# Kernel optimization log

Hardware: AMD Instinct MI355X
Metric: run time of the kernel (lower is better)

The kernel has to match this reference:

```python
import math
import jax, jax.numpy as jnp
import numpy as np


def conv2d(x, w, b, pad=0, dil=1):
    # x: [B, Cin, H, W], w: [Cout, Cin, kh, kw] (OIHW)
    y = jax.lax.conv_general_dilated(
        x, w, window_strides=(1, 1),
        padding=[(pad, pad), (pad, pad)],
        rhs_dilation=(dil, dil),
        dimension_numbers=('NCHW', 'OIHW', 'NCHW'))
    return y + b[None, :, None, None]


def setup_inputs() -> dict:
    key = jax.random.key(0)
    ks = jax.random.split(key, 8)
    B, C, H, W = 2, 64, 96, 96
    inner = 64 // 18  # = 3, as in the torch module
    n_dil = 3
    s = 0.1
    x = jax.random.normal(ks[0], (B, C, H, W), jnp.float32)
    w_red = jax.random.normal(ks[1], (inner, C, 1, 1), jnp.float32) * s
    b_red = jax.random.normal(ks[2], (inner,), jnp.float32) * s
    w_dil = jax.random.normal(ks[3], (n_dil, inner, inner, 3, 3), jnp.float32) * s
    b_dil = jax.random.normal(ks[4], (n_dil, inner), jnp.float32) * s
    w_fuse = jax.random.normal(ks[5], (C, inner * n_dil * 6, 1, 1), jnp.float32) * s
    b_fuse = jax.random.normal(ks[6], (C,), jnp.float32) * s
    return {"x": x, "w_red": w_red, "b_red": b_red, "w_dil": w_dil,
            "b_dil": b_dil, "w_fuse": w_fuse, "b_fuse": b_fuse}


def _c4_transforms(x):
    # identity, flip-W, flip-H, rot90 k=1,2,3 over spatial dims
    return [x,
            jnp.flip(x, axis=-1),
            jnp.flip(x, axis=-2),
            jnp.rot90(x, 1, axes=(2, 3)),
            jnp.rot90(x, 2, axes=(2, 3)),
            jnp.rot90(x, 3, axes=(2, 3))]


def reference(x, w_red, b_red, w_dil, b_dil, w_fuse, b_fuse):
    dilations = (1, 2, 3)
    residual_scale = 0.2
    B, C, H, W = x.shape
    x_red = conv2d(x, w_red, b_red)                    # [B, inner, H, W]
    tfs = _c4_transforms(x_red)
    feats = []
    for i, d in enumerate(dilations):
        co = conv2d(x_red, w_dil[i], b_dil[i], pad=d, dil=d)
        for tf in tfs:
            feats.append(co * tf)
    cat = jnp.concatenate(feats, axis=1)               # [B, inner*18, H, W]
    fused = conv2d(cat, w_fuse, b_fuse)                # [B, C, H, W]
    tokens = fused.reshape(B, C, H * W).transpose(0, 2, 1)  # [B, N, C]
    # Chunked attention in the original is mathematically full self-attention
    scores = jnp.einsum('bnc,bmc->bnm', tokens, tokens) / math.sqrt(C)
    attn = jax.nn.softmax(scores, axis=-1)
    out = jnp.einsum('bnm,bmc->bnc', attn, tokens)     # [B, N, C]
    out = out.transpose(0, 2, 1).reshape(B, C, H, W)
    return x + residual_scale * out
```

## Files before the change

### kernel.cpp

```cpp
#include <hip/hip_runtime.h>

#define HW    96
#define NPIX  9216
#define NCH   64
#define INNER 3
#define NDIL  3
#define BB    2
#define TOTPIX (BB * NPIX)
#define NT32  (NPIX / 32)

typedef __attribute__((ext_vector_type(8))) short short8;
typedef __attribute__((ext_vector_type(8))) unsigned short ushort8;
typedef __attribute__((ext_vector_type(4))) float f32x4;
typedef __attribute__((ext_vector_type(4))) unsigned int uint32x4;

__device__ __forceinline__ ushort f2bf_rne(float f) {
    unsigned u = __float_as_uint(f);
    u += 0x7fffu + ((u >> 16) & 1u);
    return (ushort)(u >> 16);
}
__device__ __forceinline__ float bf2f(ushort u) {
    return __uint_as_float((unsigned)u << 16);
}
__device__ __forceinline__ unsigned pack_bf(float lo, float hi) {
    return __builtin_amdgcn_perm(__float_as_uint(hi), __float_as_uint(lo), 0x07060302u);
}

__global__ __launch_bounds__(256) void
k_reduce(const float* __restrict__ x, const float* __restrict__ w_red,
         const float* __restrict__ b_red, float* __restrict__ xred) {
    __shared__ float part[4][3][64];
    int tid = threadIdx.x;
    int cp = tid >> 6, lane = tid & 63;
    int pix = blockIdx.x * 64 + lane;
    int b = pix / NPIX, n = pix % NPIX;
    const float* xb = x + (size_t)b * NCH * NPIX + (size_t)(cp * 16) * NPIX + n;
    float a0 = 0.f, a1 = 0.f, a2 = 0.f;
    #pragma unroll
    for (int c = 0; c < 16; ++c) {
        float xv = xb[(size_t)c * NPIX];
        a0 = fmaf(w_red[0 * NCH + cp * 16 + c], xv, a0);
        a1 = fmaf(w_red[1 * NCH + cp * 16 + c], xv, a1);
        a2 = fmaf(w_red[2 * NCH + cp * 16 + c], xv, a2);
    }
    part[cp][0][lane] = a0; part[cp][1][lane] = a1; part[cp][2][lane] = a2;
    __syncthreads();
    if (tid < 192) {
        int o = tid >> 6, lp = tid & 63;
        float s = ((part[0][o][lp] + part[1][o][lp]) +
                   (part[2][o][lp] + part[3][o][lp])) + b_red[o];
        int pix2 = blockIdx.x * 64 + lp;
        int b2 = pix2 / NPIX, n2 = pix2 % NPIX;
        xred[((size_t)b2 * INNER + o) * NPIX + n2] = s;
    }
}

__global__ __launch_bounds__(256) void
k_feat(const float* __restrict__ xred, const float* __restrict__ w_dil,
       const float* __restrict__ b_dil, ushort* __restrict__ FT) {
    int gid = blockIdx.x * 256 + threadIdx.x;
    int io = gid / TOTPIX;
    int pix = gid - io * TOTPIX;
    int i3 = io / 3, o = io - 3 * i3;
    int b = pix / NPIX, n = pix % NPIX;
    int h = n / HW, w = n % HW;
    const float* xr = xred + (size_t)b * INNER * NPIX;
    int d = i3 + 1;

    float co = b_dil[i3 * 3 + o];
    #pragma unroll
    for (int ci = 0; ci < 3; ++ci) {
        const float* xo = xr + ci * NPIX;
        #pragma unroll
        for (int kh = 0; kh < 3; ++kh) {
            int hh = h + (kh - 1) * d;
            #pragma unroll
            for (int kw = 0; kw < 3; ++kw) {
                int ww = w + (kw - 1) * d;
                float v = ((unsigned)hh < HW && (unsigned)ww < HW) ? xo[hh * HW + ww] : 0.f;
                co = fmaf(w_dil[(9 * i3 + 3 * o + ci) * 9 + kh * 3 + kw], v, co);
            }
        }
    }

    const float* xo = xr + o * NPIX;
    float tf0 = xo[h * HW + w];
    float tf1 = xo[h * HW + (HW - 1 - w)];
    float tf2 = xo[(HW - 1 - h) * HW + w];
    float tf3 = xo[w * HW + (HW - 1 - h)];
    float tf4 = xo[(HW - 1 - h) * HW + (HW - 1 - w)];
    float tf5 = xo[(HW - 1 - w) * HW + h];

    size_t base = (size_t)(i3 * 18 + o) * TOTPIX + pix;
    FT[base + (size_t)(0 * 3) * TOTPIX] = f2bf_rne(co * tf0);
    FT[base + (size_t)(1 * 3) * TOTPIX] = f2bf_rne(co * tf1);
    FT[base + (size_t)(2 * 3) * TOTPIX] = f2bf_rne(co * tf2);
    FT[base + (size_t)(3 * 3) * TOTPIX] = f2bf_rne(co * tf3);
    FT[base + (size_t)(4 * 3) * TOTPIX] = f2bf_rne(co * tf4);
    FT[base + (size_t)(5 * 3) * TOTPIX] = f2bf_rne(co * tf5);
}

__global__ __launch_bounds__(256) void
k_fuse(const ushort* __restrict__ FT, const float* __restrict__ w_fuse,
       const float* __restrict__ b_fuse, ushort* __restrict__ tok,
       ushort* __restrict__ tokTt) {
    __shared__ ushort wpad[64 * 72];
    __shared__ float  bsh[64];
    __shared__ ushort tile[64 * 72];

    int tid = threadIdx.x;
    for (int i = tid; i < 64 * 64; i += 256) {
        int c = i >> 6, j = i & 63;
        wpad[c * 72 + j] = (j < 54) ? f2bf_rne(w_fuse[c * 54 + j]) : (ushort)0;
    }
    if (tid < 64) bsh[tid] = b_fuse[tid];
    __syncthreads();

    int wv = tid >> 6, lane = tid & 63, quad = lane >> 4, l15 = lane & 15;
    int px0 = blockIdx.x * 64;

    short8 af[4][2];
    #pragma unroll
    for (int m = 0; m < 4; ++m)
        #pragma unroll
        for (int kc = 0; kc < 2; ++kc)
            af[m][kc] = *(const short8*)&wpad[(16 * m + l15) * 72 + quad * 8 + 32 * kc];

    f32x4 acc[4];
    #pragma unroll
    for (int m = 0; m < 4; ++m) acc[m] = (f32x4){0.f, 0.f, 0.f, 0.f};

    int px = px0 + wv * 16 + l15;
    #pragma unroll
    for (int kc = 0; kc < 2; ++kc) {
        short8 bf;
        #pragma unroll
        for (int jj = 0; jj < 8; ++jj)
            bf[jj] = (short)FT[(size_t)(quad * 8 + jj + 32 * kc) * TOTPIX + px];
        #pragma unroll
        for (int m = 0; m < 4; ++m)
            acc[m] = __builtin_amdgcn_mfma_f32_16x16x32_bf16(af[m][kc], bf, acc[m], 0, 0, 0);
    }

    #pragma unroll
    for (int m = 0; m < 4; ++m)
        #pragma unroll
        for (int r = 0; r < 4; ++r) {
            int c = 16 * m + quad * 4 + r;
            tile[c * 72 + wv * 16 + l15] = f2bf_rne(acc[m][r] + bsh[c]);
        }
    __syncthreads();

    int b0 = px0 / NPIX, n0 = px0 % NPIX;
    {
        int lp = tid >> 2, part = tid & 3;
        ushort row[16];
        #pragma unroll
        for (int k = 0; k < 16; ++k) row[k] = tile[(part * 16 + k) * 72 + lp];
        ushort* dst = tok + ((size_t)b0 * NPIX + n0 + lp) * NCH + part * 16;
        *(ushort8*)&dst[0] = *(const ushort8*)&row[0];
        *(ushort8*)&dst[8] = *(const ushort8*)&row[8];
    }
    {
        int c = tid >> 2, seg = tid & 3;
        int n = n0 + seg * 16;
        size_t base = (((size_t)b0 * NT32 + (n >> 5)) * 64 + c) * 32 + (n & 31);
        *(ushort8*)&tokTt[base]     = *(const ushort8*)&tile[c * 72 + seg * 16];
        *(ushort8*)&tokTt[base + 8] = *(const ushort8*)&tile[c * 72 + seg * 16 + 8];
    }
}

__global__ __launch_bounds__(256, 4) void
k_attn(const ushort* __restrict__ tok, const ushort* __restrict__ tokTt,
       float* __restrict__ pl, ushort* __restrict__ pacc, int P, int KP) {
    __shared__ ushort ldsK[2][32 * 72];
    __shared__ ushort ldsV[2][64 * 40];

    const int QW = NPIX / 128;
    int bid = blockIdx.x;
    int qc = bid % QW; int rest = bid / QW;
    int p = rest % P;  int b = rest / P;
    int tid = threadIdx.x;
    int wv = tid >> 6, lane = tid & 63;
    int quad = lane >> 4, l15 = lane & 15;

    const ushort* tb  = tok + (size_t)b * NPIX * NCH;
    const ushort* tvb = tokTt + (size_t)b * NT32 * (64 * 32);
    int qwave = qc * 128 + wv * 32;

    int sk_off = (tid >> 3) * 72 + (tid & 7) * 8;
    int svj = tid & 3;
    int sv_b0 = (tid >> 2) * 40 + 8 * ((2 * svj) & 3) + 4 * (svj >> 1);
    int sv_b1 = (tid >> 2) * 40 + 8 * ((2 * svj + 1) & 3) + 4 * (svj >> 1);

    short8 qf[2][2];
    const float scale = 0.125f * 1.44269504088896340736f;
    #pragma unroll
    for (int n = 0; n < 2; ++n) {
        const ushort* qr = tb + (size_t)(qwave + 16 * n + l15) * NCH + quad * 8;
        #pragma unroll
        for (int kc = 0; kc < 2; ++kc) {
            ushort8 raw = *(const ushort8*)(qr + 32 * kc);
            short8 f;
            #pragma unroll
            for (int e = 0; e < 8; ++e) f[e] = (short)f2bf_rne(bf2f(raw[e]) * scale);
            qf[n][kc] = f;
        }
    }

    f32x4 O[4][2];
    #pragma unroll
    for (int m = 0; m < 4; ++m)
        #pragma unroll
        for (int n = 0; n < 2; ++n) O[m][n] = (f32x4){0.f, 0.f, 0.f, 0.f};
    float lrun[2] = {0.f, 0.f};

    const float FM = 16.0f;
    int k0 = p * KP;
    int nt = KP / 32;

    {
        ushort8 gK = *(const ushort8*)(tb + (size_t)k0 * NCH + tid * 8);
        ushort8 gV = *(const ushort8*)(tvb + ((size_t)(k0 >> 5)) * 2048 + tid * 8);
        *(ushort8*)&ldsK[0][sk_off] = gK;
        uint32x4 v4 = *(uint32x4*)&gV;
        *(uint2*)&ldsV[0][sv_b0] = make_uint2(v4.x, v4.y);
        *(uint2*)&ldsV[0][sv_b1] = make_uint2(v4.z, v4.w);
    }
    __syncthreads();

    for (int t = 0; t < nt; ++t) {
        int cur = t & 1;
        int kbase = k0 + t * 32;
        bool pre = (t + 1 < nt);

        ushort8 nK, nV;
        if (pre) {
            nK = *(const ushort8*)(tb + (size_t)(kbase + 32) * NCH + tid * 8);
            nV = *(const ushort8*)(tvb + ((size_t)((kbase + 32) >> 5)) * 2048 + tid * 8);
        }

        short8 kd[4];
        #pragma unroll
        for (int m2 = 0; m2 < 2; ++m2)
            #pragma unroll
            for (int kc = 0; kc < 2; ++kc)
                kd[2 * m2 + kc] = *(const short8*)&ldsK[cur][(16 * m2 + l15) * 72 +
                                                            quad * 8 + 32 * kc];

        f32x4 S[2][2];
        #pragma unroll
        for (int m = 0; m < 2; ++m)
            #pragma unroll
            for (int n = 0; n < 2; ++n) S[m][n] = (f32x4){0.f, 0.f, 0.f, 0.f};

        __builtin_amdgcn_s_setprio(1);
        #pragma unroll
        for (int m2 = 0; m2 < 2; ++m2)
            #pragma unroll
            for (int cc = 0; cc < 2; ++cc)
                #pragma unroll
                for (int n = 0; n < 2; ++n)
                    S[m2][n] = __builtin_amdgcn_mfma_f32_16x16x32_bf16(kd[2 * m2 + cc],
                                                                       qf[n][cc], S[m2][n],
                                                                       0, 0, 0);
        __builtin_amdgcn_s_setprio(0);

        if (pre) {
            *(ushort8*)&ldsK[cur ^ 1][sk_off] = nK;
            uint32x4 v4 = *(uint32x4*)&nV;
            *(uint2*)&ldsV[cur ^ 1][sv_b0] = make_uint2(v4.x, v4.y);
            *(uint2*)&ldsV[cur ^ 1][sv_b1] = make_uint2(v4.z, v4.w);
        }

        short8 vf[4];
        #pragma unroll
        for (int mc = 0; mc < 4; ++mc)
            vf[mc] = *(const short8*)&ldsV[cur][(16 * mc + l15) * 40 + quad * 8];

        #pragma unroll
        for (int n = 0; n < 2; ++n) {
            float e00 = __builtin_amdgcn_exp2f(S[0][n][0] - FM);
            float e01 = __builtin_amdgcn_exp2f(S[0][n][1] - FM);
            float e02 = __builtin_amdgcn_exp2f(S[0][n][2] - FM);
            float e03 = __builtin_amdgcn_exp2f(S[0][n][3] - FM);
            float e10 = __builtin_amdgcn_exp2f(S[1][n][0] - FM);
            float e11 = __builtin_amdgcn_exp2f(S[1][n][1] - FM);
            float e12 = __builtin_amdgcn_exp2f(S[1][n][2] - FM);
            float e13 = __builtin_amdgcn_exp2f(S[1][n][3] - FM);
            lrun[n] += ((e00 + e01) + (e02 + e03)) + ((e10 + e11) + (e12 + e13));
            uint32x4 w;
            w.x = pack_bf(e00, e01); w.y = pack_bf(e02, e03);
            w.z = pack_bf(e10, e11); w.w = pack_bf(e12, e13);
            short8 bfr = *(short8*)&w;

            __builtin_amdgcn_s_setprio(1);
            #pragma unroll
            for (int mc = 0; mc < 4; ++mc)
                O[mc][n] = __builtin_amdgcn_mfma_f32_16x16x32_bf16(vf[mc], bfr,
                                                                   O[mc][n], 0, 0, 0);
            __builtin_amdgcn_s_setprio(0);
        }

        __syncthreads();
    }

    #pragma unroll
    for (int n = 0; n < 2; ++n) {
        lrun[n] += __shfl_xor(lrun[n], 16, 64);
        lrun[n] += __shfl_xor(lrun[n], 32, 64);
    }
    size_t bp = (size_t)b * P + p;
    if (quad == 0) {
        #pragma unroll
        for (int n = 0; n < 2; ++n)
            pl[bp * NPIX + qwave + 16 * n + l15] = lrun[n];
    }
    #pragma unroll
    for (int n = 0; n < 2; ++n) {
        int qg = qwave + 16 * n + l15;
        #pragma unroll
        for (int m = 0; m < 4; ++m) {
            #pragma unroll
            for (int r = 0; r < 4; ++r) {
                int c = 16 * m + quad * 4 + r;
                pacc[(bp * NCH + c) * NPIX + qg] = f2bf_rne(O[m][n][r]);
            }
        }
    }
}

__global__ void k_norm(const float* __restrict__ pl, float* __restrict__ linv, int P) {
    int idx = blockIdx.x * blockDim.x + threadIdx.x;
    if (idx >= TOTPIX) return;
    int b = idx / NPIX, n = idx % NPIX;
    float L = 0.f;
    for (int p = 0; p < P; ++p) L += pl[((size_t)b * P + p) * NPIX + n];
    linv[idx] = 0.2f / L;
}

__global__ void k_combine(const float* __restrict__ x, const float* __restrict__ linv,
                          const ushort* __restrict__ pacc, float* __restrict__ out,
                          int P) {
    int gid = blockIdx.x * blockDim.x + threadIdx.x;
    if (gid >= BB * NCH * (NPIX / 8)) return;
    int seg = gid % (NPIX / 8);
    int bc  = gid / (NPIX / 8);
    int b = bc / NCH;
    int n0 = seg * 8;
    float o[8] = {0.f, 0.f, 0.f, 0.f, 0.f, 0.f, 0.f, 0.f};
    for (int p = 0; p < P; ++p) {
        ushort8 t = *(const ushort8*)(pacc +
            (((size_t)b * P + p) * NCH + (bc % NCH)) * NPIX + n0);
        #pragma unroll
        for (int e = 0; e < 8; ++e) o[e] += bf2f(t[e]);
    }
    const float* lv = linv + (size_t)b * NPIX + n0;
    const float* xb = x + (size_t)bc * NPIX + n0;
    float* ob = out + (size_t)bc * NPIX + n0;
    #pragma unroll
    for (int e = 0; e < 8; ++e)
        ob[e] = fmaf(lv[e], o[e], xb[e]);
}

extern "C" void kernel_launch(void* const* d_in, const int* in_sizes, int n_in,
                              void* d_out, int out_size, void* d_ws, size_t ws_size,
                              hipStream_t stream) {
    const float* x      = (const float*)d_in[0];
    const float* w_red  = (const float*)d_in[1];
    const float* b_red  = (const float*)d_in[2];
    const float* w_dil  = (const float*)d_in[3];
    const float* b_dil  = (const float*)d_in[4];
    const float* w_fuse = (const float*)d_in[5];
    const float* b_fuse = (const float*)d_in[6];
    float* out = (float*)d_out;

    const size_t XRED_N = (size_t)BB * INNER * NPIX;
    const size_t FT_N   = (size_t)64 * TOTPIX;
    const size_t TOK_N  = (size_t)BB * NPIX * NCH;
    const size_t HEAD_B = XRED_N * 4 + (FT_N + 2 * TOK_N) * 2 + TOTPIX * 4;
    int P = 0;
    const int cands[5] = {16, 8, 4, 2, 1};
    for (int ci = 0; ci < 5; ++ci) {
        int cp = cands[ci];
        size_t need = HEAD_B + (size_t)BB * cp * NPIX * (4 + NCH * 2);
        if (ws_size >= need) { P = cp; break; }
    }
    if (P == 0) return;

    float*  xred  = (float*)d_ws;
    ushort* FT    = (ushort*)(xred + XRED_N);
    ushort* tok   = FT + FT_N;
    ushort* tokTt = tok + TOK_N;
    float*  pl    = (float*)(tokTt + TOK_N);
    float*  linv  = pl + (size_t)BB * P * NPIX;
    ushort* pacc  = (ushort*)(linv + TOTPIX);

    k_reduce <<<TOTPIX / 64, 256, 0, stream>>>(x, w_red, b_red, xred);
    k_feat   <<<9 * TOTPIX / 256, 256, 0, stream>>>(xred, w_dil, b_dil, FT);
    k_fuse   <<<TOTPIX / 64, 256, 0, stream>>>(FT, w_fuse, b_fuse, tok, tokTt);
    k_attn   <<<BB * P * (NPIX / 128), 256, 0, stream>>>(tok, tokTt, pl, pacc,
                                                         P, NPIX / P);
    k_norm   <<<(TOTPIX + 255) / 256, 256, 0, stream>>>(pl, linv, P);
    k_combine<<<(BB * NCH * (NPIX / 8) + 255) / 256, 256, 0, stream>>>(x, linv, pacc,
                                                                       out, P);
}
```

Baseline: 146.0 us.

## Interleave QK/exp per tile half, atomically accumulate row sums, drop norm kernel

Restructures the attention inner loop so each 16-key half of the score tile is computed and exponentiated right away, which shortens the live range of score registers. Launch bounds are raised to 5 waves per SIMD, and key/value pointers are advanced incrementally. Per-split row sums are now atomically added into one buffer, cleared by a memset, so the separate normalisation kernel is removed and the reciprocal moves into the combine kernel. The exchange is atomic contention on the sum buffer and an extra memset launch, while one kernel launch and the partial-sum buffer go away.

Measured after the change: 143.7 us. About the same (-1.6%).

```diff
diff --git a/kernel.cpp b/kernel.cpp
--- a/kernel.cpp
+++ b/kernel.cpp
@@ -170,9 +170,9 @@
     }
 }
 
-__global__ __launch_bounds__(256, 4) void
+__global__ __launch_bounds__(256, 5) void
 k_attn(const ushort* __restrict__ tok, const ushort* __restrict__ tokTt,
-       float* __restrict__ pl, ushort* __restrict__ pacc, int P, int KP) {
+       float* __restrict__ L, ushort* __restrict__ pacc, int P, int KP) {
     __shared__ ushort ldsK[2][32 * 72];
     __shared__ ushort ldsV[2][64 * 40];
 
@@ -214,14 +214,18 @@
         #pragma unroll
         for (int n = 0; n < 2; ++n) O[m][n] = (f32x4){0.f, 0.f, 0.f, 0.f};
     float lrun[2] = {0.f, 0.f};
+    const f32x4 Zc = (f32x4){0.f, 0.f, 0.f, 0.f};
 
     const float FM = 16.0f;
     int k0 = p * KP;
     int nt = KP / 32;
 
+    const ushort* pK = tb + (size_t)k0 * NCH + tid * 8;
+    const ushort* pV = tvb + ((size_t)(k0 >> 5)) * 2048 + tid * 8;
+
     {
-        ushort8 gK = *(const ushort8*)(tb + (size_t)k0 * NCH + tid * 8);
-        ushort8 gV = *(const ushort8*)(tvb + ((size_t)(k0 >> 5)) * 2048 + tid * 8);
+        ushort8 gK = *(const ushort8*)pK;
+        ushort8 gV = *(const ushort8*)pV;
         *(ushort8*)&ldsK[0][sk_off] = gK;
         uint32x4 v4 = *(uint32x4*)&gV;
         *(uint2*)&ldsV[0][sv_b0] = make_uint2(v4.x, v4.y);
@@ -231,13 +235,13 @@
 
     for (int t = 0; t < nt; ++t) {
         int cur = t & 1;
-        int kbase = k0 + t * 32;
         bool pre = (t + 1 < nt);
+        pK += 32 * NCH;  pV += 2048;
 
         ushort8 nK, nV;
         if (pre) {
-            nK = *(const ushort8*)(tb + (size_t)(kbase + 32) * NCH + tid * 8);
-            nV = *(const ushort8*)(tvb + ((size_t)((kbase + 32) >> 5)) * 2048 + tid * 8);
+            nK = *(const ushort8*)pK;
+            nV = *(const ushort8*)pV;
         }
 
         short8 kd[4];
@@ -248,23 +252,33 @@
                 kd[2 * m2 + kc] = *(const short8*)&ldsK[cur][(16 * m2 + l15) * 72 +
                                                             quad * 8 + 32 * kc];
 
-        f32x4 S[2][2];
-        #pragma unroll
-        for (int m = 0; m < 2; ++m)
-            #pragma unroll
-            for (int n = 0; n < 2; ++n) S[m][n] = (f32x4){0.f, 0.f, 0.f, 0.f};
-
-        __builtin_amdgcn_s_setprio(1);
-        #pragma unroll
-        for (int m2 = 0; m2 < 2; ++m2)
-            #pragma unroll
-            for (int cc = 0; cc < 2; ++cc)
-                #pragma unroll
-                for (int n = 0; n < 2; ++n)
-                    S[m2][n] = __builtin_amdgcn_mfma_f32_16x16x32_bf16(kd[2 * m2 + cc],
-                                                                       qf[n][cc], S[m2][n],
-                                                                       0, 0, 0);
-        __builtin_amdgcn_s_setprio(0);
+        uint32x4 wac[2];
+        #pragma unroll
+        for (int m2 = 0; m2 < 2; ++m2) {
+            f32x4 Sm[2];
+            __builtin_amdgcn_s_setprio(1);
+            #pragma unroll
+            for (int n = 0; n < 2; ++n) {
+                Sm[n] = __builtin_amdgcn_mfma_f32_16x16x32_bf16(kd[2 * m2 + 0],
+                                                                qf[n][0], Zc, 0, 0, 0);
+                Sm[n] = __builtin_amdgcn_mfma_f32_16x16x32_bf16(kd[2 * m2 + 1],
+                                                                qf[n][1], Sm[n], 0, 0, 0);
+            }
+            __builtin_amdgcn_s_setprio(0);
+            #pragma unroll
+            for (int n = 0; n < 2; ++n) {
+                float e0 = __builtin_amdgcn_exp2f(Sm[n][0] - FM);
+                float e1 = __builtin_amdgcn_exp2f(Sm[n][1] - FM);
+                float e2 = __builtin_amdgcn_exp2f(Sm[n][2] - FM);
+                float e3 = __builtin_amdgcn_exp2f(Sm[n][3] - FM);
+                lrun[n] += (e0 + e1) + (e2 + e3);
+                if (m2 == 0) {
+                    wac[n].x = pack_bf(e0, e1); wac[n].y = pack_bf(e2, e3);
+                } else {
+                    wac[n].z = pack_bf(e0, e1); wac[n].w = pack_bf(e2, e3);
+                }
+            }
+        }
 
         if (pre) {
             *(ushort8*)&ldsK[cur ^ 1][sk_off] = nK;
@@ -278,29 +292,16 @@
         for (int mc = 0; mc < 4; ++mc)
             vf[mc] = *(const short8*)&ldsV[cur][(16 * mc + l15) * 40 + quad * 8];
 
+        __builtin_amdgcn_s_setprio(1);
         #pragma unroll
         for (int n = 0; n < 2; ++n) {
-            float e00 = __builtin_amdgcn_exp2f(S[0][n][0] - FM);
-            float e01 = __builtin_amdgcn_exp2f(S[0][n][1] - FM);
-            float e02 = __builtin_amdgcn_exp2f(S[0][n][2] - FM);
-            float e03 = __builtin_amdgcn_exp2f(S[0][n][3] - FM);
-            float e10 = __builtin_amdgcn_exp2f(S[1][n][0] - FM);
-            float e11 = __builtin_amdgcn_exp2f(S[1][n][1] - FM);
-            float e12 = __builtin_amdgcn_exp2f(S[1][n][2] - FM);
-            float e13 = __builtin_amdgcn_exp2f(S[1][n][3] - FM);
-            lrun[n] += ((e00 + e01) + (e02 + e03)) + ((e10 + e11) + (e12 + e13));
-            uint32x4 w;
-            w.x = pack_bf(e00, e01); w.y = pack_bf(e02, e03);
-            w.z = pack_bf(e10, e11); w.w = pack_bf(e12, e13);
-            short8 bfr = *(short8*)&w;
-
-            __builtin_amdgcn_s_setprio(1);
+            short8 bfr = *(short8*)&wac[n];
             #pragma unroll
             for (int mc = 0; mc < 4; ++mc)
                 O[mc][n] = __builtin_amdgcn_mfma_f32_16x16x32_bf16(vf[mc], bfr,
                                                                    O[mc][n], 0, 0, 0);
-            __builtin_amdgcn_s_setprio(0);
-        }
+        }
+        __builtin_amdgcn_s_setprio(0);
 
         __syncthreads();
     }
@@ -310,12 +311,12 @@
         lrun[n] += __shfl_xor(lrun[n], 16, 64);
         lrun[n] += __shfl_xor(lrun[n], 32, 64);
     }
+    if (quad == 0) {
+        #pragma unroll
+        for (int n = 0; n < 2; ++n)
+            atomicAdd(&L[(size_t)b * NPIX + qwave + 16 * n + l15], lrun[n]);
+    }
     size_t bp = (size_t)b * P + p;
-    if (quad == 0) {
-        #pragma unroll
-        for (int n = 0; n < 2; ++n)
-            pl[bp * NPIX + qwave + 16 * n + l15] = lrun[n];
-    }
     #pragma unroll
     for (int n = 0; n < 2; ++n) {
         int qg = qwave + 16 * n + l15;
@@ -330,16 +331,7 @@
     }
 }
 
-__global__ void k_norm(const float* __restrict__ pl, float* __restrict__ linv, int P) {
-    int idx = blockIdx.x * blockDim.x + threadIdx.x;
-    if (idx >= TOTPIX) return;
-    int b = idx / NPIX, n = idx % NPIX;
-    float L = 0.f;
-    for (int p = 0; p < P; ++p) L += pl[((size_t)b * P + p) * NPIX + n];
-    linv[idx] = 0.2f / L;
-}
-
-__global__ void k_combine(const float* __restrict__ x, const float* __restrict__ linv,
+__global__ void k_combine(const float* __restrict__ x, const float* __restrict__ L,
                           const ushort* __restrict__ pacc, float* __restrict__ out,
                           int P) {
     int gid = blockIdx.x * blockDim.x + threadIdx.x;
@@ -355,12 +347,12 @@
         #pragma unroll
         for (int e = 0; e < 8; ++e) o[e] += bf2f(t[e]);
     }
-    const float* lv = linv + (size_t)b * NPIX + n0;
+    const float* lv = L + (size_t)b * NPIX + n0;
     const float* xb = x + (size_t)bc * NPIX + n0;
     float* ob = out + (size_t)bc * NPIX + n0;
     #pragma unroll
     for (int e = 0; e < 8; ++e)
-        ob[e] = fmaf(lv[e], o[e], xb[e]);
+        ob[e] = fmaf(0.2f / lv[e], o[e], xb[e]);
 }
 
 extern "C" void kernel_launch(void* const* d_in, const int* in_sizes, int n_in,
@@ -383,7 +375,7 @@
     const int cands[5] = {16, 8, 4, 2, 1};
     for (int ci = 0; ci < 5; ++ci) {
         int cp = cands[ci];
-        size_t need = HEAD_B + (size_t)BB * cp * NPIX * (4 + NCH * 2);
+        size_t need = HEAD_B + (size_t)BB * cp * NPIX * NCH * 2;
         if (ws_size >= need) { P = cp; break; }
     }
     if (P == 0) return;
@@ -392,16 +384,15 @@
     ushort* FT    = (ushort*)(xred + XRED_N);
     ushort* tok   = FT + FT_N;
     ushort* tokTt = tok + TOK_N;
-    float*  pl    = (float*)(tokTt + TOK_N);
-    float*  linv  = pl + (size_t)BB * P * NPIX;
-    ushort* pacc  = (ushort*)(linv + TOTPIX);
+    float*  L     = (float*)(tokTt + TOK_N);
+    ushort* pacc  = (ushort*)(L + TOTPIX);
 
     k_reduce <<<TOTPIX / 64, 256, 0, stream>>>(x, w_red, b_red, xred);
     k_feat   <<<9 * TOTPIX / 256, 256, 0, stream>>>(xred, w_dil, b_dil, FT);
+    hipMemsetAsync(L, 0, TOTPIX * sizeof(float), stream);
     k_fuse   <<<TOTPIX / 64, 256, 0, stream>>>(FT, w_fuse, b_fuse, tok, tokTt);
-    k_attn   <<<BB * P * (NPIX / 128), 256, 0, stream>>>(tok, tokTt, pl, pacc,
+    k_attn   <<<BB * P * (NPIX / 128), 256, 0, stream>>>(tok, tokTt, L, pacc,
                                                          P, NPIX / P);
-    k_norm   <<<(TOTPIX + 255) / 256, 256, 0, stream>>>(pl, linv, P);
-    k_combine<<<(BB * NCH * (NPIX / 8) + 255) / 256, 256, 0, stream>>>(x, linv, pacc,
+    k_combine<<<(BB * NCH * (NPIX / 8) + 255) / 256, 256, 0, stream>>>(x, L, pacc,
                                                                        out, P);
 }
```
